# Optimization experiments

Hardware: AMD Instinct MI355X
Metric: run time of the kernel (lower is better)

## Reference

```python
import jax, jax.numpy as jnp
import numpy as np
import math

IN_FEATURES = 512
RFF_FEATURES = 2048
OUT_FEATURES = 1000
N = 8192
RIDGE_PENALTY = 1.0
MEAN_FIELD_FACTOR = 25.0
RFF_SCALAR = math.sqrt(RFF_FEATURES / 2)  # 32.0


def _random_ortho(key, n, m):
    q, _ = jnp.linalg.qr(jax.random.normal(key, (n, m), dtype=jnp.float32))
    return q


def setup_inputs() -> dict:
    key = jax.random.key(0)
    k_d, k_w, k_norm, k_b, k_lw, k_lb, k_cov = jax.random.split(key, 7)
    D = jax.random.normal(k_d, (N, IN_FEATURES), dtype=jnp.float32)
    # RFF weight: concat of random orthonormal blocks (rff_features > in_features)
    ws = []
    dim_left = RFF_FEATURES
    kk = k_w
    while dim_left > IN_FEATURES:
        kk, sub = jax.random.split(kk)
        ws.append(_random_ortho(sub, IN_FEATURES, IN_FEATURES))
        dim_left -= IN_FEATURES
    kk, sub = jax.random.split(kk)
    ws.append(_random_ortho(sub, IN_FEATURES, dim_left))
    W = jnp.concatenate(ws, axis=1)  # [in, rff]
    feature_norm = jax.random.normal(k_norm, W.shape, dtype=jnp.float32) ** 2
    W = W * jnp.sqrt(feature_norm.sum(0))
    b = jax.random.uniform(k_b, (RFF_FEATURES,), dtype=jnp.float32) * (2.0 * math.pi)
    # logit head (nn.Linear): weight [out, rff], bias [out]
    bound = 1.0 / math.sqrt(RFF_FEATURES)
    logit_w = jax.random.uniform(k_lw, (OUT_FEATURES, RFF_FEATURES), dtype=jnp.float32,
                                 minval=-bound, maxval=bound)
    logit_b = jax.random.uniform(k_lb, (OUT_FEATURES,), dtype=jnp.float32,
                                 minval=-bound, maxval=bound)
    # positive-definite covariance buffer (stand-in for inverted precision)
    A = jax.random.normal(k_cov, (RFF_FEATURES, RFF_FEATURES), dtype=jnp.float32) * 0.01
    covariance = A @ A.T + jnp.eye(RFF_FEATURES, dtype=jnp.float32)
    return {"D": D, "W": W, "b": b, "logit_w": logit_w, "logit_b": logit_b,
            "covariance": covariance}


def reference(D, W, b, logit_w, logit_b, covariance):
    # RFF feature map: cos(D @ W + b) / rff_scalar  -> [N, rff]
    Phi = jnp.cos(D @ W + b) / RFF_SCALAR
    # linear head -> [N, out]
    pred = Phi @ logit_w.T + logit_b
    # diag(Phi @ cov @ Phi.T) * ridge computed row-wise in O(N*r^2)
    diag_cov = jnp.sum((Phi @ covariance) * Phi, axis=-1) * RIDGE_PENALTY  # [N]
    logits_scale = jnp.sqrt(1.0 + diag_cov * MEAN_FIELD_FACTOR)
    return pred / logits_scale[:, None]
```

## Files before the change

kernel.cpp:

```cpp
#include <hip/hip_runtime.h>
#include <hip/hip_fp8.h>
#include <math.h>

#define N_ROWS 8192
#define IN_F   512
#define RFF    2048
#define OUT_F  1000
#define OUT_PAD 1024
#define INV_RFF_SCALAR 0.03125f
#define MEAN_FIELD 25.0f
#define PHI_NT 24

typedef __attribute__((ext_vector_type(8))) short short8;
typedef __attribute__((ext_vector_type(4))) float f32x4;
typedef __attribute__((ext_vector_type(2))) long long2v;

__device__ __forceinline__ unsigned short f32_to_bf16(float f) {
    unsigned u = __float_as_uint(f);
    unsigned r = 0x7FFFu + ((u >> 16) & 1u);
    return (unsigned short)((u + r) >> 16);
}
__device__ __forceinline__ float bf16_to_f32(unsigned short h) {
    return __uint_as_float(((unsigned)h) << 16);
}
__device__ __forceinline__ unsigned char f32_to_fp8(float x) {
    __hip_fp8_e4m3 q(x);
    return (unsigned char)q.__x;
}

__device__ __forceinline__ int perm64(int k) {
    return (k & ~63) | (((k >> 3) & 3) << 4) | (((k >> 5) & 1) << 3) | (k & 7);
}

__device__ __forceinline__ void stage_tile64(const unsigned short* __restrict__ X,
                                             int r0, int k0, unsigned char* lds,
                                             int w, int lane) {
    #pragma unroll
    for (int h = 0; h < 4; ++h) {
        int qb = h * 256 + w * 64;
        int q = qb + lane;
        int rt = q >> 7, c = (q >> 4) & 7, r = q & 15;
        const void* g = X + (size_t)(r0 + rt * 16 + r) * RFF + k0 + c * 8;
        __builtin_amdgcn_global_load_lds(
            (const __attribute__((address_space(1))) void*)g,
            (__attribute__((address_space(3))) void*)(lds + qb * 16),
            16, 0, 0);
    }
}

__device__ __forceinline__ void stage_tile8(const unsigned char* __restrict__ X,
                                            int r0, int k0b, unsigned char* lds,
                                            int w, int lane) {
    #pragma unroll
    for (int h = 0; h < 4; ++h) {
        int qb = h * 256 + w * 64;
        int q = qb + lane;
        int rt = q >> 7, c = (q >> 4) & 7, r = q & 15;
        const void* g = X + (size_t)(r0 + rt * 16 + r) * RFF + k0b + c * 16;
        __builtin_amdgcn_global_load_lds(
            (const __attribute__((address_space(1))) void*)g,
            (__attribute__((address_space(3))) void*)(lds + qb * 16),
            16, 0, 0);
    }
}

__global__ __launch_bounds__(256) void conv_split_kernel(
    const float* __restrict__ X, unsigned short* __restrict__ H,
    unsigned short* __restrict__ L, int n4)
{
    int i = blockIdx.x * 256 + threadIdx.x;
    if (i >= n4) return;
    float4 v = ((const float4*)X)[i];
    ushort4 h, l;
    h.x = f32_to_bf16(v.x); l.x = f32_to_bf16(v.x - bf16_to_f32(h.x));
    h.y = f32_to_bf16(v.y); l.y = f32_to_bf16(v.y - bf16_to_f32(h.y));
    h.z = f32_to_bf16(v.z); l.z = f32_to_bf16(v.z - bf16_to_f32(h.z));
    h.w = f32_to_bf16(v.w); l.w = f32_to_bf16(v.w - bf16_to_f32(h.w));
    ((ushort4*)H)[i] = h;
    ((ushort4*)L)[i] = l;
}

__global__ __launch_bounds__(256) void conv_covu8_kernel(
    const float* __restrict__ X, unsigned char* __restrict__ O)
{
    int i = blockIdx.x * 256 + threadIdx.x;
    int base = i * 4;
    int row = base >> 11;
    int col = base & 2047;
    int bn = row >> 7, bk = col >> 7;
    float w = (bk < bn) ? 16.0f : (bk == bn ? 8.0f : 0.0f);
    float4 v = ((const float4*)X)[i];
    float w0 = (col + 0 == row) ? 0.0f : w;
    float w1 = (col + 1 == row) ? 0.0f : w;
    float w2 = (col + 2 == row) ? 0.0f : w;
    float w3 = (col + 3 == row) ? 0.0f : w;
    uchar4 o;
    o.x = f32_to_fp8(v.x * w0); o.y = f32_to_fp8(v.y * w1);
    o.z = f32_to_fp8(v.z * w2); o.w = f32_to_fp8(v.w * w3);
    *(uchar4*)(O + (size_t)row * RFF + perm64(col)) = o;
}

__global__ __launch_bounds__(256) void conv_covd_kernel(
    const float* __restrict__ X, float* __restrict__ Cd)
{
    int i = blockIdx.x * 256 + threadIdx.x;
    if (i < RFF) Cd[i] = X[(size_t)i * RFF + i];
}

__global__ __launch_bounds__(256) void conv_phi8_kernel(
    const unsigned short* __restrict__ Phi16, unsigned char* __restrict__ Phi8)
{
    int i = blockIdx.x * 256 + threadIdx.x;
    int base = i * 4;
    int row = base >> 11;
    int col = base & 2047;
    ushort4 v = ((const ushort4*)Phi16)[i];
    uchar4 o;
    o.x = f32_to_fp8(bf16_to_f32(v.x) * 32.0f);
    o.y = f32_to_fp8(bf16_to_f32(v.y) * 32.0f);
    o.z = f32_to_fp8(bf16_to_f32(v.z) * 32.0f);
    o.w = f32_to_fp8(bf16_to_f32(v.w) * 32.0f);
    *(uchar4*)(Phi8 + (size_t)row * RFF + perm64(col)) = o;
}

__global__ __launch_bounds__(256) void conv_lw_kernel(
    const float* __restrict__ Lw, unsigned short* __restrict__ O)
{
    int i = blockIdx.x * 256 + threadIdx.x;
    int base = i * 4;
    int row = base >> 11;
    ushort4 o;
    if (row < OUT_F) {
        float4 v = ((const float4*)Lw)[i];
        o.x = f32_to_bf16(v.x); o.y = f32_to_bf16(v.y);
        o.z = f32_to_bf16(v.z); o.w = f32_to_bf16(v.w);
    } else {
        o.x = o.y = o.z = o.w = 0;
    }
    ((ushort4*)O)[i] = o;
}

__global__ __launch_bounds__(256) void conv_wt_kernel(
    const float* __restrict__ W, unsigned short* __restrict__ TH,
    unsigned short* __restrict__ TL)
{
    __shared__ float tile[64][65];
    const int tid = threadIdx.x;
    const int n0 = blockIdx.x * 64;
    const int k0 = blockIdx.y * 64;
    #pragma unroll
    for (int i = 0; i < 16; ++i) {
        int e = i * 256 + tid;
        int r = e >> 6, c = e & 63;
        tile[r][c] = W[(size_t)(k0 + r) * RFF + n0 + c];
    }
    __syncthreads();
    #pragma unroll
    for (int i = 0; i < 16; ++i) {
        int e = i * 256 + tid;
        int r = e >> 6, c = e & 63;
        float v = tile[c][r];
        unsigned short h = f32_to_bf16(v);
        unsigned short l = f32_to_bf16(v - bf16_to_f32(h));
        TH[(size_t)(n0 + r) * IN_F + k0 + c] = h;
        TL[(size_t)(n0 + r) * IN_F + k0 + c] = l;
    }
}


__device__ __forceinline__ void gload16u(const void* g, unsigned short* lds) {
    __builtin_amdgcn_global_load_lds(
        (const __attribute__((address_space(1))) void*)g,
        (__attribute__((address_space(3))) void*)lds, 16, 0, 0);
}

__device__ __forceinline__ void stageA_g(const unsigned short* __restrict__ src,
                                         int r0, int kk, unsigned short* ldsbuf,
                                         int Qa, int h, int w, int lane) {
    int q   = w * 64 + lane;
    int RTl = h * 8 + Qa * 4 + (q >> 7);
    int c   = (q >> 4) & 7, r = q & 15;
    const void* g = src + (size_t)(r0 + RTl * 16 + r) * IN_F + kk + c * 8;
    int RTu = h * 8 + Qa * 4 + (w >> 1);
    int cu  = (w & 1) * 4;
    gload16u(g, ldsbuf + RTu * 1024 + cu * 128);
}

__device__ __forceinline__ void stageB_g(const unsigned short* __restrict__ src,
                                         int cc0, int kk, unsigned short* ldsbuf,
                                         int nh, int h, int w, int lane) {
    int q    = w * 64 + lane;
    int i    = q >> 7;
    int RTp  = (i >> 1) * 4 + nh * 2 + (i & 1);
    int c    = (q >> 4) & 7, r = q & 15;
    const void* g = src + (size_t)(cc0 + h * 128 + RTp * 16 + r) * IN_F + kk + c * 8;
    int iu   = w >> 1;
    int RTpu = (iu >> 1) * 4 + nh * 2 + (iu & 1);
    int RTu  = h * 8 + RTpu;
    int cu   = (w & 1) * 4;
    gload16u(g, ldsbuf + RTu * 1024 + cu * 128);
}

#define SB0() __builtin_amdgcn_sched_barrier(0)
#define BARRIER() do { SB0(); __builtin_amdgcn_s_barrier(); SB0(); } while (0)
#define WAITVM(N) do { asm volatile("s_waitcnt vmcnt(" #N ")"); SB0(); } while (0)

#define READ_FA(FA, mh) do {                                                  \
    _Pragma("unroll")                                                         \
    for (int i_ = 0; i_ < 4; ++i_) {                                          \
        FA[i_][0] = *(const short8*)(A + (wm * 8 + (mh) * 4 + i_) * 1024      \
                                       + quad * 128 + ln * 8);                \
        FA[i_][1] = *(const short8*)(A + (wm * 8 + (mh) * 4 + i_) * 1024      \
                                       + 512 + quad * 128 + ln * 8);          \
    } } while (0)

#define READ_FB(FB, nh) do {                                                  \
    _Pragma("unroll")                                                         \
    for (int j_ = 0; j_ < 2; ++j_) {                                          \
        FB[j_][0] = *(const short8*)(B + (wn * 4 + (nh) * 2 + j_) * 1024      \
                                       + quad * 128 + ln * 8);                \
        FB[j_][1] = *(const short8*)(B + (wn * 4 + (nh) * 2 + j_) * 1024      \
                                       + 512 + quad * 128 + ln * 8);          \
    } } while (0)

#define MFMA16(MH, NH, FA, FB) do {                                           \
    __builtin_amdgcn_s_setprio(1);                                            \
    _Pragma("unroll")                                                         \
    for (int s_ = 0; s_ < 2; ++s_)                                            \
        _Pragma("unroll")                                                     \
        for (int i_ = 0; i_ < 4; ++i_)                                        \
            _Pragma("unroll")                                                 \
            for (int j_ = 0; j_ < 2; ++j_)                                    \
                acc[(MH) * 4 + i_][(NH) * 2 + j_] =                           \
                    __builtin_amdgcn_mfma_f32_16x16x32_bf16(                  \
                        FA[i_][s_], FB[j_][s_],                               \
                        acc[(MH) * 4 + i_][(NH) * 2 + j_], 0, 0, 0);          \
    __builtin_amdgcn_s_setprio(0);                                            \
} while (0)

__global__ __launch_bounds__(512, 2) void phi_mfma8p_kernel(
    const unsigned short* __restrict__ Dh, const unsigned short* __restrict__ Dl,
    const unsigned short* __restrict__ Wth, const unsigned short* __restrict__ Wtl,
    const float* __restrict__ bias, unsigned short* __restrict__ Phi)
{
    __shared__ unsigned short ldsA[2 * 16384];
    __shared__ unsigned short ldsB[2 * 16384];
    const int tid = threadIdx.x;
    const int w = tid >> 6, lane = tid & 63;
    const int wm = w >> 2, wn = w & 3;
    const int quad = lane >> 4, ln = lane & 15;

    const int bid = blockIdx.x;
    const int xcd = bid & 7, idx = bid >> 3;
    const int rb = (xcd >> 1) * 8 + (idx & 7);
    const int cb = (xcd & 1) * 4 + (idx >> 3);
    const int r0 = rb * 256;
    const int c0 = cb * 256;

    f32x4 acc[8][4];
    #pragma unroll
    for (int i = 0; i < 8; ++i)
        #pragma unroll
        for (int j = 0; j < 4; ++j)
            acc[i][j] = (f32x4)(0.0f);

    stageA_g(Dh,  r0, 0, ldsA, 0, 0, w, lane);
    stageA_g(Dh,  r0, 0, ldsA, 0, 1, w, lane);
    stageA_g(Dh,  r0, 0, ldsA, 1, 0, w, lane);
    stageA_g(Dh,  r0, 0, ldsA, 1, 1, w, lane);
    stageB_g(Wth, c0, 0, ldsB, 0, 0, w, lane);
    stageB_g(Wth, c0, 0, ldsB, 0, 1, w, lane);
    stageB_g(Wth, c0, 0, ldsB, 1, 0, w, lane);
    stageB_g(Wth, c0, 0, ldsB, 1, 1, w, lane);
    stageA_g(Dh,  r0, 64, ldsA + 16384, 0, 0, w, lane);
    stageA_g(Dh,  r0, 64, ldsA + 16384, 0, 1, w, lane);
    stageB_g(Wth, c0, 64, ldsB + 16384, 0, 0, w, lane);
    stageB_g(Wth, c0, 64, ldsB + 16384, 0, 1, w, lane);
    WAITVM(4);
    BARRIER();

    for (int t = 0; t < PHI_NT - 1; ++t) {
        const int buf = t & 1;
        const unsigned short* A = ldsA + buf * 16384;
        const unsigned short* B = ldsB + buf * 16384;
        unsigned short* curA = ldsA + buf * 16384;
        unsigned short* curB = ldsB + buf * 16384;
        unsigned short* othA = ldsA + (buf ^ 1) * 16384;
        unsigned short* othB = ldsB + (buf ^ 1) * 16384;
        const bool has2 = (t + 2) < PHI_NT;
        const int k1 = (t + 1) * 64, k2 = (t + 2) * 64;
        const int kk1 = k1 & 511, kk2 = k2 & 511;
        const unsigned short* A1 = (k1 >= 1024) ? Dl : Dh;
        const unsigned short* B1 = (k1 >= 1024) ? Wth : (k1 >= 512 ? Wtl : Wth);
        const unsigned short* A2 = (k2 >= 1024) ? Dl : Dh;
        const unsigned short* B2 = (k2 >= 1024) ? Wth : (k2 >= 512 ? Wtl : Wth);

        short8 fa[4][2], fb0[2][2], fb1[2][2];

        READ_FA(fa, 0);
        READ_FB(fb0, 0);
        stageA_g(A1, r0, kk1, othA, 1, 0, w, lane);
        stageA_g(A1, r0, kk1, othA, 1, 1, w, lane);
        BARRIER();
        MFMA16(0, 0, fa, fb0);
        BARRIER();

        READ_FB(fb1, 1);
        stageB_g(B1, c0, kk1, othB, 1, 0, w, lane);
        stageB_g(B1, c0, kk1, othB, 1, 1, w, lane);
        BARRIER();
        MFMA16(0, 1, fa, fb1);
        BARRIER();

        READ_FA(fa, 1);
        if (has2) { stageA_g(A2, r0, kk2, curA, 0, 0, w, lane);
                    stageA_g(A2, r0, kk2, curA, 0, 1, w, lane); }
        BARRIER();
        MFMA16(1, 0, fa, fb0);
        BARRIER();

        if (has2) { stageB_g(B2, c0, kk2, curB, 0, 0, w, lane);
                    stageB_g(B2, c0, kk2, curB, 0, 1, w, lane);
                    WAITVM(4); }
        else      { WAITVM(0); }
        BARRIER();
        MFMA16(1, 1, fa, fb1);
        BARRIER();
    }

    {
        asm volatile("" ::: "memory");
        const unsigned short* A = ldsA + ((PHI_NT - 1) & 1) * 16384;
        const unsigned short* B = ldsB + ((PHI_NT - 1) & 1) * 16384;
        short8 fa[4][2], fb0[2][2], fb1[2][2];
        READ_FA(fa, 0);
        READ_FB(fb0, 0);
        READ_FB(fb1, 1);
        MFMA16(0, 0, fa, fb0);
        MFMA16(0, 1, fa, fb1);
        READ_FA(fa, 1);
        MFMA16(1, 0, fa, fb0);
        MFMA16(1, 1, fa, fb1);
    }

    float bv[4];
    #pragma unroll
    for (int nt = 0; nt < 4; ++nt)
        bv[nt] = bias[c0 + wn * 64 + nt * 16 + ln];
    #pragma unroll
    for (int mt = 0; mt < 8; ++mt)
        #pragma unroll
        for (int nt = 0; nt < 4; ++nt) {
            int col = c0 + wn * 64 + nt * 16 + ln;
            #pragma unroll
            for (int reg = 0; reg < 4; ++reg) {
                int row = r0 + wm * 128 + mt * 16 + quad * 4 + reg;
                float z = acc[mt][nt][reg] + bv[nt];
                float p = __cosf(z) * INV_RFF_SCALAR;
                Phi[(size_t)row * RFF + col] = f32_to_bf16(p);
            }
        }
}

__global__ __launch_bounds__(256) void diag8_kernel(
    const unsigned char* __restrict__ Phi8, const unsigned char* __restrict__ CovU8,
    const unsigned short* __restrict__ Phi16, const float* __restrict__ Cd,
    float* __restrict__ diag)
{
    __shared__ __align__(16) unsigned char ldsA[16384];
    __shared__ __align__(16) unsigned char ldsB[16384];
    const int tid = threadIdx.x;
    const int w = tid >> 6, lane = tid & 63;
    const int wm = w >> 1, wn = w & 1;
    const int quad = lane >> 4, ln = lane & 15;
    const int J = 15 - blockIdx.x;
    const int r0 = blockIdx.y * 128;
    const int c0 = J * 128;
    const int kmax = (J + 1) * 128;

    f32x4 acc[4][4];
    #pragma unroll
    for (int i = 0; i < 4; ++i)
        #pragma unroll
        for (int j = 0; j < 4; ++j)
            acc[i][j] = (f32x4)(0.0f);

    for (int k0 = 0; k0 < kmax; k0 += 128) {
        __syncthreads();
        stage_tile8(Phi8,  r0, k0, ldsA, w, lane);
        stage_tile8(CovU8, c0, k0, ldsB, w, lane);
        __syncthreads();

        #pragma unroll
        for (int kb = 0; kb < 2; ++kb) {
            long2v fa[4], fb[4];
            #pragma unroll
            for (int t = 0; t < 4; ++t) {
                fa[t] = *(const long2v*)(ldsA + (((wm * 4 + t) * 128 + (kb * 4 + quad) * 16 + ln) << 4));
                fb[t] = *(const long2v*)(ldsB + (((wn * 4 + t) * 128 + (kb * 4 + quad) * 16 + ln) << 4));
            }
            #pragma unroll
            for (int mt = 0; mt < 4; ++mt)
                #pragma unroll
                for (int nt = 0; nt < 4; ++nt)
                    acc[mt][nt] = __builtin_amdgcn_mfma_f32_16x16x32_fp8_fp8(
                        fa[mt].x, fb[nt].x, acc[mt][nt], 0, 0, 0);
            #pragma unroll
            for (int mt = 0; mt < 4; ++mt)
                #pragma unroll
                for (int nt = 0; nt < 4; ++nt)
                    acc[mt][nt] = __builtin_amdgcn_mfma_f32_16x16x32_fp8_fp8(
                        fa[mt].y, fb[nt].y, acc[mt][nt], 0, 0, 0);
        }
    }

    float cd[4];
    #pragma unroll
    for (int nt = 0; nt < 4; ++nt)
        cd[nt] = 256.0f * Cd[c0 + wn * 64 + nt * 16 + ln];
    #pragma unroll
    for (int mt = 0; mt < 4; ++mt) {
        float psum[4] = {0.f, 0.f, 0.f, 0.f};
        #pragma unroll
        for (int nt = 0; nt < 4; ++nt) {
            int col = c0 + wn * 64 + nt * 16 + ln;
            #pragma unroll
            for (int reg = 0; reg < 4; ++reg) {
                int row = r0 + wm * 64 + mt * 16 + quad * 4 + reg;
                float pv = bf16_to_f32(Phi16[(size_t)row * RFF + col]);
                psum[reg] = fmaf(fmaf(cd[nt], pv, acc[mt][nt][reg]), pv, psum[reg]);
            }
        }
        #pragma unroll
        for (int off = 1; off < 16; off <<= 1)
            #pragma unroll
            for (int reg = 0; reg < 4; ++reg)
                psum[reg] += __shfl_xor(psum[reg], off, 16);
        if (ln == 0) {
            #pragma unroll
            for (int reg = 0; reg < 4; ++reg) {
                int row = r0 + wm * 64 + mt * 16 + quad * 4 + reg;
                atomicAdd(&diag[row], psum[reg] * (1.0f / 256.0f));
            }
        }
    }
}

__global__ __launch_bounds__(256) void pred_mfma_kernel(
    const unsigned short* __restrict__ Phi, const unsigned short* __restrict__ Lw,
    const float* __restrict__ Lb, const float* __restrict__ diag,
    float* __restrict__ out)
{
    __shared__ __align__(16) unsigned char ldsA[16384];
    __shared__ __align__(16) unsigned char ldsB[16384];
    const int tid = threadIdx.x;
    const int w = tid >> 6, lane = tid & 63;
    const int wm = w >> 1, wn = w & 1;
    const int quad = lane >> 4, ln = lane & 15;
    const int r0 = blockIdx.y * 128;
    const int c0 = blockIdx.x * 128;

    f32x4 acc[4][4];
    #pragma unroll
    for (int i = 0; i < 4; ++i)
        #pragma unroll
        for (int j = 0; j < 4; ++j)
            acc[i][j] = (f32x4)(0.0f);

    for (int k0 = 0; k0 < RFF; k0 += 64) {
        __syncthreads();
        stage_tile64(Phi, r0, k0, ldsA, w, lane);
        stage_tile64(Lw,  c0, k0, ldsB, w, lane);
        __syncthreads();

        #pragma unroll
        for (int s = 0; s < 2; ++s) {
            short8 fa[4], fb[4];
            #pragma unroll
            for (int t = 0; t < 4; ++t) {
                fa[t] = *(const short8*)(ldsA + (((wm * 4 + t) * 128 + (s * 4 + quad) * 16 + ln) << 4));
                fb[t] = *(const short8*)(ldsB + (((wn * 4 + t) * 128 + (s * 4 + quad) * 16 + ln) << 4));
            }
            #pragma unroll
            for (int mt = 0; mt < 4; ++mt)
                #pragma unroll
                for (int nt = 0; nt < 4; ++nt)
                    acc[mt][nt] = __builtin_amdgcn_mfma_f32_16x16x32_bf16(
                        fa[mt], fb[nt], acc[mt][nt], 0, 0, 0);
        }
    }

    #pragma unroll
    for (int mt = 0; mt < 4; ++mt) {
        float s[4];
        #pragma unroll
        for (int reg = 0; reg < 4; ++reg) {
            int row = r0 + wm * 64 + mt * 16 + quad * 4 + reg;
            s[reg] = 1.0f / sqrtf(1.0f + MEAN_FIELD * diag[row]);
        }
        #pragma unroll
        for (int nt = 0; nt < 4; ++nt) {
            int col = c0 + wn * 64 + nt * 16 + ln;
            if (col < OUT_F) {
                float bv = Lb[col];
                #pragma unroll
                for (int reg = 0; reg < 4; ++reg) {
                    int row = r0 + wm * 64 + mt * 16 + quad * 4 + reg;
                    out[(size_t)row * OUT_F + col] = (acc[mt][nt][reg] + bv) * s[reg];
                }
            }
        }
    }
}

extern "C" void kernel_launch(void* const* d_in, const int* in_sizes, int n_in,
                              void* d_out, int out_size, void* d_ws, size_t ws_size,
                              hipStream_t stream) {
    const float* D    = (const float*)d_in[0];
    const float* W    = (const float*)d_in[1];
    const float* bias = (const float*)d_in[2];
    const float* Lw   = (const float*)d_in[3];
    const float* Lb   = (const float*)d_in[4];
    const float* cov  = (const float*)d_in[5];
    float* out = (float*)d_out;

    char* p = (char*)d_ws;
    unsigned short* Phi16 = (unsigned short*)p;  p += (size_t)N_ROWS * RFF * 2;
    unsigned char*  Phi8  = (unsigned char*)p;
    unsigned short* Dh    = (unsigned short*)p;  p += (size_t)N_ROWS * IN_F * 2;
    unsigned short* Dl    = (unsigned short*)p;  p += (size_t)N_ROWS * IN_F * 2;
    unsigned short* Wth   = (unsigned short*)p;  p += (size_t)RFF * IN_F * 2;
    unsigned short* Wtl   = (unsigned short*)p;  p += (size_t)RFF * IN_F * 2;
    unsigned short* Lw16  = (unsigned short*)p;  p += (size_t)OUT_PAD * RFF * 2;
    unsigned char*  CovU8 = (unsigned char*)p;
    float*          Cd    = (float*)(p + (size_t)RFF * RFF);
    p += (size_t)RFF * RFF * 2;
    float* diag           = (float*)p;

    hipMemsetAsync(diag, 0, N_ROWS * sizeof(float), stream);

    dim3 blk(256);
    conv_split_kernel<<<dim3((N_ROWS * IN_F / 4 + 255) / 256), blk, 0, stream>>>(D, Dh, Dl, N_ROWS * IN_F / 4);
    conv_wt_kernel<<<dim3(RFF / 64, IN_F / 64), blk, 0, stream>>>(W, Wth, Wtl);
    conv_lw_kernel<<<dim3(OUT_PAD * RFF / 4 / 256), blk, 0, stream>>>(Lw, Lw16);
    conv_covu8_kernel<<<dim3(RFF * RFF / 4 / 256), blk, 0, stream>>>(cov, CovU8);
    conv_covd_kernel<<<dim3(RFF / 256), blk, 0, stream>>>(cov, Cd);

    phi_mfma8p_kernel<<<dim3(256), dim3(512), 0, stream>>>(Dh, Dl, Wth, Wtl, bias, Phi16);
    conv_phi8_kernel<<<dim3(N_ROWS * RFF / 4 / 256), blk, 0, stream>>>(Phi16, Phi8);

    diag8_kernel<<<dim3(16, N_ROWS / 128), blk, 0, stream>>>(Phi8, CovU8, Phi16, Cd, diag);
    pred_mfma_kernel<<<dim3(OUT_PAD / 128, N_ROWS / 128), blk, 0, stream>>>(Phi16, Lw16, Lb, diag, out);
}
```

Baseline: 313.7 us.

## Rewrite pred GEMM as 8-wave double-buffered pipelined kernel with XCD-aware tiling

Replaces the simple single-buffered 256-thread pred GEMM with a 512-thread, 256x128-tile kernel. It double-buffers LDS, interleaves the global-to-LDS loads for step t+2 with MFMA phases, and raises MFMA priority via setprio. Blocks are remapped so row tiles cluster per XCD for L2 reuse. The goal is to hide load latency and remove the two full syncthreads per k-step, at the cost of more complex scheduling and higher LDS use.

```diff
diff --git a/kernel.cpp b/kernel.cpp
--- a/kernel.cpp
+++ b/kernel.cpp
@@ -10,6 +10,7 @@
 #define INV_RFF_SCALAR 0.03125f
 #define MEAN_FIELD 25.0f
 #define PHI_NT 24
+#define PRED_NT 32
 
 typedef __attribute__((ext_vector_type(8))) short short8;
 typedef __attribute__((ext_vector_type(4))) float f32x4;
@@ -30,22 +31,6 @@
 
 __device__ __forceinline__ int perm64(int k) {
     return (k & ~63) | (((k >> 3) & 3) << 4) | (((k >> 5) & 1) << 3) | (k & 7);
-}
-
-__device__ __forceinline__ void stage_tile64(const unsigned short* __restrict__ X,
-                                             int r0, int k0, unsigned char* lds,
-                                             int w, int lane) {
-    #pragma unroll
-    for (int h = 0; h < 4; ++h) {
-        int qb = h * 256 + w * 64;
-        int q = qb + lane;
-        int rt = q >> 7, c = (q >> 4) & 7, r = q & 15;
-        const void* g = X + (size_t)(r0 + rt * 16 + r) * RFF + k0 + c * 8;
-        __builtin_amdgcn_global_load_lds(
-            (const __attribute__((address_space(1))) void*)g,
-            (__attribute__((address_space(3))) void*)(lds + qb * 16),
-            16, 0, 0);
-    }
 }
 
 __device__ __forceinline__ void stage_tile8(const unsigned char* __restrict__ X,
@@ -174,13 +159,14 @@
         (__attribute__((address_space(3))) void*)lds, 16, 0, 0);
 }
 
-__device__ __forceinline__ void stageA_g(const unsigned short* __restrict__ src,
-                                         int r0, int kk, unsigned short* ldsbuf,
+__device__ __forceinline__ void stage_ab(const unsigned short* __restrict__ src,
+                                         int stride, int r0v, int kk,
+                                         unsigned short* ldsbuf,
                                          int Qa, int h, int w, int lane) {
     int q   = w * 64 + lane;
-    int RTl = h * 8 + Qa * 4 + (q >> 7);
+    int RT  = h * 8 + Qa * 4 + (q >> 7);
     int c   = (q >> 4) & 7, r = q & 15;
-    const void* g = src + (size_t)(r0 + RTl * 16 + r) * IN_F + kk + c * 8;
+    const void* g = src + (size_t)(r0v + RT * 16 + r) * stride + kk + c * 8;
     int RTu = h * 8 + Qa * 4 + (w >> 1);
     int cu  = (w & 1) * 4;
     gload16u(g, ldsbuf + RTu * 1024 + cu * 128);
@@ -204,6 +190,7 @@
 #define SB0() __builtin_amdgcn_sched_barrier(0)
 #define BARRIER() do { SB0(); __builtin_amdgcn_s_barrier(); SB0(); } while (0)
 #define WAITVM(N) do { asm volatile("s_waitcnt vmcnt(" #N ")"); SB0(); } while (0)
+
 
 #define READ_FA(FA, mh) do {                                                  \
     _Pragma("unroll")                                                         \
@@ -264,16 +251,16 @@
         for (int j = 0; j < 4; ++j)
             acc[i][j] = (f32x4)(0.0f);
 
-    stageA_g(Dh,  r0, 0, ldsA, 0, 0, w, lane);
-    stageA_g(Dh,  r0, 0, ldsA, 0, 1, w, lane);
-    stageA_g(Dh,  r0, 0, ldsA, 1, 0, w, lane);
-    stageA_g(Dh,  r0, 0, ldsA, 1, 1, w, lane);
+    stage_ab(Dh, IN_F, r0, 0, ldsA, 0, 0, w, lane);
+    stage_ab(Dh, IN_F, r0, 0, ldsA, 0, 1, w, lane);
+    stage_ab(Dh, IN_F, r0, 0, ldsA, 1, 0, w, lane);
+    stage_ab(Dh, IN_F, r0, 0, ldsA, 1, 1, w, lane);
     stageB_g(Wth, c0, 0, ldsB, 0, 0, w, lane);
     stageB_g(Wth, c0, 0, ldsB, 0, 1, w, lane);
     stageB_g(Wth, c0, 0, ldsB, 1, 0, w, lane);
     stageB_g(Wth, c0, 0, ldsB, 1, 1, w, lane);
-    stageA_g(Dh,  r0, 64, ldsA + 16384, 0, 0, w, lane);
-    stageA_g(Dh,  r0, 64, ldsA + 16384, 0, 1, w, lane);
+    stage_ab(Dh, IN_F, r0, 64, ldsA + 16384, 0, 0, w, lane);
+    stage_ab(Dh, IN_F, r0, 64, ldsA + 16384, 0, 1, w, lane);
     stageB_g(Wth, c0, 64, ldsB + 16384, 0, 0, w, lane);
     stageB_g(Wth, c0, 64, ldsB + 16384, 0, 1, w, lane);
     WAITVM(4);
@@ -299,8 +286,8 @@
 
         READ_FA(fa, 0);
         READ_FB(fb0, 0);
-        stageA_g(A1, r0, kk1, othA, 1, 0, w, lane);
-        stageA_g(A1, r0, kk1, othA, 1, 1, w, lane);
+        stage_ab(A1, IN_F, r0, kk1, othA, 1, 0, w, lane);
+        stage_ab(A1, IN_F, r0, kk1, othA, 1, 1, w, lane);
         BARRIER();
         MFMA16(0, 0, fa, fb0);
         BARRIER();
@@ -313,8 +300,8 @@
         BARRIER();
 
         READ_FA(fa, 1);
-        if (has2) { stageA_g(A2, r0, kk2, curA, 0, 0, w, lane);
-                    stageA_g(A2, r0, kk2, curA, 0, 1, w, lane); }
+        if (has2) { stage_ab(A2, IN_F, r0, kk2, curA, 0, 0, w, lane);
+                    stage_ab(A2, IN_F, r0, kk2, curA, 0, 1, w, lane); }
         BARRIER();
         MFMA16(1, 0, fa, fb0);
         BARRIER();
@@ -446,19 +433,58 @@
     }
 }
 
-__global__ __launch_bounds__(256) void pred_mfma_kernel(
+
+#define READ_FA2(FA, mh) do {                                                 \
+    _Pragma("unroll")                                                         \
+    for (int i_ = 0; i_ < 2; ++i_) {                                          \
+        FA[i_][0] = *(const short8*)(A + (wm * 4 + (mh) * 2 + i_) * 1024      \
+                                       + quad * 128 + ln * 8);                \
+        FA[i_][1] = *(const short8*)(A + (wm * 4 + (mh) * 2 + i_) * 1024      \
+                                       + 512 + quad * 128 + ln * 8);          \
+    } } while (0)
+
+#define READ_FB2(FB, nh) do {                                                 \
+    _Pragma("unroll")                                                         \
+    for (int j_ = 0; j_ < 2; ++j_) {                                          \
+        FB[j_][0] = *(const short8*)(B + (wn * 4 + (nh) * 2 + j_) * 1024      \
+                                       + quad * 128 + ln * 8);                \
+        FB[j_][1] = *(const short8*)(B + (wn * 4 + (nh) * 2 + j_) * 1024      \
+                                       + 512 + quad * 128 + ln * 8);          \
+    } } while (0)
+
+#define MFMA8(MH, NH, FA, FB) do {                                            \
+    __builtin_amdgcn_s_setprio(1);                                            \
+    _Pragma("unroll")                                                         \
+    for (int s_ = 0; s_ < 2; ++s_)                                            \
+        _Pragma("unroll")                                                     \
+        for (int i_ = 0; i_ < 2; ++i_)                                        \
+            _Pragma("unroll")                                                 \
+            for (int j_ = 0; j_ < 2; ++j_)                                    \
+                acc[(MH) * 2 + i_][(NH) * 2 + j_] =                           \
+                    __builtin_amdgcn_mfma_f32_16x16x32_bf16(                  \
+                        FA[i_][s_], FB[j_][s_],                               \
+                        acc[(MH) * 2 + i_][(NH) * 2 + j_], 0, 0, 0);          \
+    __builtin_amdgcn_s_setprio(0);                                            \
+} while (0)
+
+__global__ __launch_bounds__(512, 2) void pred_mfma8p_kernel(
     const unsigned short* __restrict__ Phi, const unsigned short* __restrict__ Lw,
     const float* __restrict__ Lb, const float* __restrict__ diag,
     float* __restrict__ out)
 {
-    __shared__ __align__(16) unsigned char ldsA[16384];
-    __shared__ __align__(16) unsigned char ldsB[16384];
+    __shared__ unsigned short ldsA[2 * 16384];
+    __shared__ unsigned short ldsB[2 * 8192];
     const int tid = threadIdx.x;
     const int w = tid >> 6, lane = tid & 63;
     const int wm = w >> 1, wn = w & 1;
     const int quad = lane >> 4, ln = lane & 15;
-    const int r0 = blockIdx.y * 128;
-    const int c0 = blockIdx.x * 128;
+
+    const int bid = blockIdx.x;
+    const int xcd = bid & 7, idx = bid >> 3;
+    const int rb = xcd * 4 + (idx >> 3);
+    const int cb = idx & 7;
+    const int r0 = rb * 256;
+    const int c0 = cb * 128;
 
     f32x4 acc[4][4];
     #pragma unroll
@@ -467,27 +493,74 @@
         for (int j = 0; j < 4; ++j)
             acc[i][j] = (f32x4)(0.0f);
 
-    for (int k0 = 0; k0 < RFF; k0 += 64) {
-        __syncthreads();
-        stage_tile64(Phi, r0, k0, ldsA, w, lane);
-        stage_tile64(Lw,  c0, k0, ldsB, w, lane);
-        __syncthreads();
-
-        #pragma unroll
-        for (int s = 0; s < 2; ++s) {
-            short8 fa[4], fb[4];
-            #pragma unroll
-            for (int t = 0; t < 4; ++t) {
-                fa[t] = *(const short8*)(ldsA + (((wm * 4 + t) * 128 + (s * 4 + quad) * 16 + ln) << 4));
-                fb[t] = *(const short8*)(ldsB + (((wn * 4 + t) * 128 + (s * 4 + quad) * 16 + ln) << 4));
-            }
-            #pragma unroll
-            for (int mt = 0; mt < 4; ++mt)
-                #pragma unroll
-                for (int nt = 0; nt < 4; ++nt)
-                    acc[mt][nt] = __builtin_amdgcn_mfma_f32_16x16x32_bf16(
-                        fa[mt], fb[nt], acc[mt][nt], 0, 0, 0);
-        }
+    stage_ab(Phi, RFF, r0, 0, ldsA, 0, 0, w, lane);
+    stage_ab(Phi, RFF, r0, 0, ldsA, 1, 0, w, lane);
+    stage_ab(Phi, RFF, r0, 0, ldsA, 0, 1, w, lane);
+    stage_ab(Phi, RFF, r0, 0, ldsA, 1, 1, w, lane);
+    stage_ab(Lw,  RFF, c0, 0, ldsB, 0, 0, w, lane);
+    stage_ab(Lw,  RFF, c0, 0, ldsB, 1, 0, w, lane);
+    stage_ab(Phi, RFF, r0, 64, ldsA + 16384, 0, 0, w, lane);
+    stage_ab(Phi, RFF, r0, 64, ldsA + 16384, 1, 0, w, lane);
+    stage_ab(Phi, RFF, r0, 64, ldsA + 16384, 0, 1, w, lane);
+    stage_ab(Phi, RFF, r0, 64, ldsA + 16384, 1, 1, w, lane);
+    stage_ab(Lw,  RFF, c0, 64, ldsB + 8192, 0, 0, w, lane);
+    stage_ab(Lw,  RFF, c0, 64, ldsB + 8192, 1, 0, w, lane);
+    WAITVM(6);
+    BARRIER();
+
+    for (int t = 0; t < PRED_NT - 1; ++t) {
+        const int buf = t & 1;
+        const unsigned short* A = ldsA + buf * 16384;
+        const unsigned short* B = ldsB + buf * 8192;
+        unsigned short* curA = ldsA + buf * 16384;
+        unsigned short* curB = ldsB + buf * 8192;
+        const bool has2 = (t + 2) < PRED_NT;
+        const int kk2 = (t + 2) * 64;
+
+        short8 fa0[2][2], fa1[2][2], fb0[2][2], fb1[2][2];
+
+        READ_FA2(fa0, 0);
+        READ_FB2(fb0, 0);
+        BARRIER();
+        MFMA8(0, 0, fa0, fb0);
+        BARRIER();
+
+        READ_FB2(fb1, 1);
+        BARRIER();
+        MFMA8(0, 1, fa0, fb1);
+        BARRIER();
+
+        READ_FA2(fa1, 1);
+        if (has2) { stage_ab(Lw, RFF, c0, kk2, curB, 0, 0, w, lane);
+                    stage_ab(Lw, RFF, c0, kk2, curB, 1, 0, w, lane); }
+        BARRIER();
+        MFMA8(1, 0, fa1, fb0);
+        BARRIER();
+
+        if (has2) { stage_ab(Phi, RFF, r0, kk2, curA, 0, 0, w, lane);
+                    stage_ab(Phi, RFF, r0, kk2, curA, 1, 0, w, lane);
+                    stage_ab(Phi, RFF, r0, kk2, curA, 0, 1, w, lane);
+                    stage_ab(Phi, RFF, r0, kk2, curA, 1, 1, w, lane);
+                    WAITVM(6); }
+        else      { WAITVM(0); }
+        BARRIER();
+        MFMA8(1, 1, fa1, fb1);
+        BARRIER();
+    }
+
+    {
+        asm volatile("" ::: "memory");
+        const unsigned short* A = ldsA + ((PRED_NT - 1) & 1) * 16384;
+        const unsigned short* B = ldsB + ((PRED_NT - 1) & 1) * 8192;
+        short8 fa0[2][2], fa1[2][2], fb0[2][2], fb1[2][2];
+        READ_FA2(fa0, 0);
+        READ_FB2(fb0, 0);
+        READ_FB2(fb1, 1);
+        READ_FA2(fa1, 1);
+        MFMA8(0, 0, fa0, fb0);
+        MFMA8(0, 1, fa0, fb1);
+        MFMA8(1, 0, fa1, fb0);
+        MFMA8(1, 1, fa1, fb1);
     }
 
     #pragma unroll
@@ -550,5 +623,5 @@
     conv_phi8_kernel<<<dim3(N_ROWS * RFF / 4 / 256), blk, 0, stream>>>(Phi16, Phi8);
 
     diag8_kernel<<<dim3(16, N_ROWS / 128), blk, 0, stream>>>(Phi8, CovU8, Phi16, Cd, diag);
-    pred_mfma_kernel<<<dim3(OUT_PAD / 128, N_ROWS / 128), blk, 0, stream>>>(Phi16, Lw16, Lb, diag, out);
-}
+    pred_mfma8p_kernel<<<dim3(256), dim3(512), 0, stream>>>(Phi16, Lw16, Lb, diag, out);
+}
```

After: 325.8 us. +3.9%, slower.

## Double-buffer LDS staging in diag and pred GEMM kernels with XCD-aware tiling

Applied to the files above, without the earlier changes.

The diag8 kernel now double-buffers its fp8 tiles: it prefetches the next K tile into the alternate LDS buffer while the MFMAs run on the current one, and it raises wave priority around the MFMA block. The pred kernel is rewritten as a 512-thread, 256x128 tile kernel with double-buffered global_load_lds staging, a per-XCD block-to-tile mapping and priority hints. The aim is to hide global load latency and cut the two __syncthreads per iteration. The cost is doubled LDS per block and fewer concurrent blocks.

```diff
diff --git a/kernel.cpp b/kernel.cpp
--- a/kernel.cpp
+++ b/kernel.cpp
@@ -10,6 +10,7 @@
 #define INV_RFF_SCALAR 0.03125f
 #define MEAN_FIELD 25.0f
 #define PHI_NT 24
+#define PRED_NT 32
 
 typedef __attribute__((ext_vector_type(8))) short short8;
 typedef __attribute__((ext_vector_type(4))) float f32x4;
@@ -30,22 +31,6 @@
 
 __device__ __forceinline__ int perm64(int k) {
     return (k & ~63) | (((k >> 3) & 3) << 4) | (((k >> 5) & 1) << 3) | (k & 7);
-}
-
-__device__ __forceinline__ void stage_tile64(const unsigned short* __restrict__ X,
-                                             int r0, int k0, unsigned char* lds,
-                                             int w, int lane) {
-    #pragma unroll
-    for (int h = 0; h < 4; ++h) {
-        int qb = h * 256 + w * 64;
-        int q = qb + lane;
-        int rt = q >> 7, c = (q >> 4) & 7, r = q & 15;
-        const void* g = X + (size_t)(r0 + rt * 16 + r) * RFF + k0 + c * 8;
-        __builtin_amdgcn_global_load_lds(
-            (const __attribute__((address_space(1))) void*)g,
-            (__attribute__((address_space(3))) void*)(lds + qb * 16),
-            16, 0, 0);
-    }
 }
 
 __device__ __forceinline__ void stage_tile8(const unsigned char* __restrict__ X,
@@ -174,13 +159,14 @@
         (__attribute__((address_space(3))) void*)lds, 16, 0, 0);
 }
 
-__device__ __forceinline__ void stageA_g(const unsigned short* __restrict__ src,
-                                         int r0, int kk, unsigned short* ldsbuf,
+__device__ __forceinline__ void stage_ab(const unsigned short* __restrict__ src,
+                                         int stride, int r0v, int kk,
+                                         unsigned short* ldsbuf,
                                          int Qa, int h, int w, int lane) {
     int q   = w * 64 + lane;
-    int RTl = h * 8 + Qa * 4 + (q >> 7);
+    int RT  = h * 8 + Qa * 4 + (q >> 7);
     int c   = (q >> 4) & 7, r = q & 15;
-    const void* g = src + (size_t)(r0 + RTl * 16 + r) * IN_F + kk + c * 8;
+    const void* g = src + (size_t)(r0v + RT * 16 + r) * stride + kk + c * 8;
     int RTu = h * 8 + Qa * 4 + (w >> 1);
     int cu  = (w & 1) * 4;
     gload16u(g, ldsbuf + RTu * 1024 + cu * 128);
@@ -204,6 +190,7 @@
 #define SB0() __builtin_amdgcn_sched_barrier(0)
 #define BARRIER() do { SB0(); __builtin_amdgcn_s_barrier(); SB0(); } while (0)
 #define WAITVM(N) do { asm volatile("s_waitcnt vmcnt(" #N ")"); SB0(); } while (0)
+
 
 #define READ_FA(FA, mh) do {                                                  \
     _Pragma("unroll")                                                         \
@@ -264,16 +251,16 @@
         for (int j = 0; j < 4; ++j)
             acc[i][j] = (f32x4)(0.0f);
 
-    stageA_g(Dh,  r0, 0, ldsA, 0, 0, w, lane);
-    stageA_g(Dh,  r0, 0, ldsA, 0, 1, w, lane);
-    stageA_g(Dh,  r0, 0, ldsA, 1, 0, w, lane);
-    stageA_g(Dh,  r0, 0, ldsA, 1, 1, w, lane);
+    stage_ab(Dh, IN_F, r0, 0, ldsA, 0, 0, w, lane);
+    stage_ab(Dh, IN_F, r0, 0, ldsA, 0, 1, w, lane);
+    stage_ab(Dh, IN_F, r0, 0, ldsA, 1, 0, w, lane);
+    stage_ab(Dh, IN_F, r0, 0, ldsA, 1, 1, w, lane);
     stageB_g(Wth, c0, 0, ldsB, 0, 0, w, lane);
     stageB_g(Wth, c0, 0, ldsB, 0, 1, w, lane);
     stageB_g(Wth, c0, 0, ldsB, 1, 0, w, lane);
     stageB_g(Wth, c0, 0, ldsB, 1, 1, w, lane);
-    stageA_g(Dh,  r0, 64, ldsA + 16384, 0, 0, w, lane);
-    stageA_g(Dh,  r0, 64, ldsA + 16384, 0, 1, w, lane);
+    stage_ab(Dh, IN_F, r0, 64, ldsA + 16384, 0, 0, w, lane);
+    stage_ab(Dh, IN_F, r0, 64, ldsA + 16384, 0, 1, w, lane);
     stageB_g(Wth, c0, 64, ldsB + 16384, 0, 0, w, lane);
     stageB_g(Wth, c0, 64, ldsB + 16384, 0, 1, w, lane);
     WAITVM(4);
@@ -299,8 +286,8 @@
 
         READ_FA(fa, 0);
         READ_FB(fb0, 0);
-        stageA_g(A1, r0, kk1, othA, 1, 0, w, lane);
-        stageA_g(A1, r0, kk1, othA, 1, 1, w, lane);
+        stage_ab(A1, IN_F, r0, kk1, othA, 1, 0, w, lane);
+        stage_ab(A1, IN_F, r0, kk1, othA, 1, 1, w, lane);
         BARRIER();
         MFMA16(0, 0, fa, fb0);
         BARRIER();
@@ -313,8 +300,8 @@
         BARRIER();
 
         READ_FA(fa, 1);
-        if (has2) { stageA_g(A2, r0, kk2, curA, 0, 0, w, lane);
-                    stageA_g(A2, r0, kk2, curA, 0, 1, w, lane); }
+        if (has2) { stage_ab(A2, IN_F, r0, kk2, curA, 0, 0, w, lane);
+                    stage_ab(A2, IN_F, r0, kk2, curA, 0, 1, w, lane); }
         BARRIER();
         MFMA16(1, 0, fa, fb0);
         BARRIER();
@@ -362,13 +349,13 @@
         }
 }
 
-__global__ __launch_bounds__(256) void diag8_kernel(
+__global__ __launch_bounds__(256, 2) void diag8_kernel(
     const unsigned char* __restrict__ Phi8, const unsigned char* __restrict__ CovU8,
     const unsigned short* __restrict__ Phi16, const float* __restrict__ Cd,
     float* __restrict__ diag)
 {
-    __shared__ __align__(16) unsigned char ldsA[16384];
-    __shared__ __align__(16) unsigned char ldsB[16384];
+    __shared__ __align__(16) unsigned char ldsA[2 * 16384];
+    __shared__ __align__(16) unsigned char ldsB[2 * 16384];
     const int tid = threadIdx.x;
     const int w = tid >> 6, lane = tid & 63;
     const int wm = w >> 1, wn = w & 1;
@@ -385,19 +372,30 @@
         for (int j = 0; j < 4; ++j)
             acc[i][j] = (f32x4)(0.0f);
 
-    for (int k0 = 0; k0 < kmax; k0 += 128) {
-        __syncthreads();
-        stage_tile8(Phi8,  r0, k0, ldsA, w, lane);
-        stage_tile8(CovU8, c0, k0, ldsB, w, lane);
-        __syncthreads();
-
+    stage_tile8(Phi8,  r0, 0, ldsA, w, lane);
+    stage_tile8(CovU8, c0, 0, ldsB, w, lane);
+    WAITVM(0);
+    BARRIER();
+
+    int it = 0;
+    for (int k0 = 0; k0 < kmax; k0 += 128, ++it) {
+        const int buf = it & 1;
+        const unsigned char* A = ldsA + buf * 16384;
+        const unsigned char* B = ldsB + buf * 16384;
+
+        if (k0 + 128 < kmax) {
+            stage_tile8(Phi8,  r0, k0 + 128, ldsA + (buf ^ 1) * 16384, w, lane);
+            stage_tile8(CovU8, c0, k0 + 128, ldsB + (buf ^ 1) * 16384, w, lane);
+        }
+
+        __builtin_amdgcn_s_setprio(1);
         #pragma unroll
         for (int kb = 0; kb < 2; ++kb) {
             long2v fa[4], fb[4];
             #pragma unroll
             for (int t = 0; t < 4; ++t) {
-                fa[t] = *(const long2v*)(ldsA + (((wm * 4 + t) * 128 + (kb * 4 + quad) * 16 + ln) << 4));
-                fb[t] = *(const long2v*)(ldsB + (((wn * 4 + t) * 128 + (kb * 4 + quad) * 16 + ln) << 4));
+                fa[t] = *(const long2v*)(A + (((wm * 4 + t) * 128 + (kb * 4 + quad) * 16 + ln) << 4));
+                fb[t] = *(const long2v*)(B + (((wn * 4 + t) * 128 + (kb * 4 + quad) * 16 + ln) << 4));
             }
             #pragma unroll
             for (int mt = 0; mt < 4; ++mt)
@@ -412,6 +410,10 @@
                     acc[mt][nt] = __builtin_amdgcn_mfma_f32_16x16x32_fp8_fp8(
                         fa[mt].y, fb[nt].y, acc[mt][nt], 0, 0, 0);
         }
+        __builtin_amdgcn_s_setprio(0);
+
+        WAITVM(0);
+        BARRIER();
     }
 
     float cd[4];
@@ -446,19 +448,24 @@
     }
 }
 
-__global__ __launch_bounds__(256) void pred_mfma_kernel(
+__global__ __launch_bounds__(512, 2) void pred_min2_kernel(
     const unsigned short* __restrict__ Phi, const unsigned short* __restrict__ Lw,
     const float* __restrict__ Lb, const float* __restrict__ diag,
     float* __restrict__ out)
 {
-    __shared__ __align__(16) unsigned char ldsA[16384];
-    __shared__ __align__(16) unsigned char ldsB[16384];
+    __shared__ unsigned short ldsA[2 * 16384];
+    __shared__ unsigned short ldsB[2 * 8192];
     const int tid = threadIdx.x;
     const int w = tid >> 6, lane = tid & 63;
     const int wm = w >> 1, wn = w & 1;
     const int quad = lane >> 4, ln = lane & 15;
-    const int r0 = blockIdx.y * 128;
-    const int c0 = blockIdx.x * 128;
+
+    const int bid = blockIdx.x;
+    const int xcd = bid & 7, idx = bid >> 3;
+    const int rb = xcd * 4 + (idx >> 3);
+    const int cb = idx & 7;
+    const int r0 = rb * 256;
+    const int c0 = cb * 128;
 
     f32x4 acc[4][4];
     #pragma unroll
@@ -467,27 +474,56 @@
         for (int j = 0; j < 4; ++j)
             acc[i][j] = (f32x4)(0.0f);
 
-    for (int k0 = 0; k0 < RFF; k0 += 64) {
-        __syncthreads();
-        stage_tile64(Phi, r0, k0, ldsA, w, lane);
-        stage_tile64(Lw,  c0, k0, ldsB, w, lane);
-        __syncthreads();
-
-        #pragma unroll
-        for (int s = 0; s < 2; ++s) {
-            short8 fa[4], fb[4];
-            #pragma unroll
-            for (int t = 0; t < 4; ++t) {
-                fa[t] = *(const short8*)(ldsA + (((wm * 4 + t) * 128 + (s * 4 + quad) * 16 + ln) << 4));
-                fb[t] = *(const short8*)(ldsB + (((wn * 4 + t) * 128 + (s * 4 + quad) * 16 + ln) << 4));
-            }
-            #pragma unroll
-            for (int mt = 0; mt < 4; ++mt)
+    stage_ab(Phi, RFF, r0, 0, ldsA, 0, 0, w, lane);
+    stage_ab(Phi, RFF, r0, 0, ldsA, 1, 0, w, lane);
+    stage_ab(Phi, RFF, r0, 0, ldsA, 0, 1, w, lane);
+    stage_ab(Phi, RFF, r0, 0, ldsA, 1, 1, w, lane);
+    stage_ab(Lw,  RFF, c0, 0, ldsB, 0, 0, w, lane);
+    stage_ab(Lw,  RFF, c0, 0, ldsB, 1, 0, w, lane);
+    WAITVM(0);
+    BARRIER();
+
+    for (int t = 0; t < PRED_NT; ++t) {
+        const int buf = t & 1;
+        const unsigned short* A = ldsA + buf * 16384;
+        const unsigned short* B = ldsB + buf * 8192;
+
+        if (t + 1 < PRED_NT) {
+            const int kk = (t + 1) * 64;
+            unsigned short* nA = ldsA + (buf ^ 1) * 16384;
+            unsigned short* nB = ldsB + (buf ^ 1) * 8192;
+            stage_ab(Phi, RFF, r0, kk, nA, 0, 0, w, lane);
+            stage_ab(Phi, RFF, r0, kk, nA, 1, 0, w, lane);
+            stage_ab(Phi, RFF, r0, kk, nA, 0, 1, w, lane);
+            stage_ab(Phi, RFF, r0, kk, nA, 1, 1, w, lane);
+            stage_ab(Lw,  RFF, c0, kk, nB, 0, 0, w, lane);
+            stage_ab(Lw,  RFF, c0, kk, nB, 1, 0, w, lane);
+        }
+
+        short8 fa[4][2], fb[4][2];
+        #pragma unroll
+        for (int i_ = 0; i_ < 4; ++i_) {
+            fa[i_][0] = *(const short8*)(A + (wm * 4 + i_) * 1024 + quad * 128 + ln * 8);
+            fa[i_][1] = *(const short8*)(A + (wm * 4 + i_) * 1024 + 512 + quad * 128 + ln * 8);
+        }
+        #pragma unroll
+        for (int j_ = 0; j_ < 4; ++j_) {
+            fb[j_][0] = *(const short8*)(B + (wn * 4 + j_) * 1024 + quad * 128 + ln * 8);
+            fb[j_][1] = *(const short8*)(B + (wn * 4 + j_) * 1024 + 512 + quad * 128 + ln * 8);
+        }
+        __builtin_amdgcn_s_setprio(1);
+        #pragma unroll
+        for (int s_ = 0; s_ < 2; ++s_)
+            #pragma unroll
+            for (int i_ = 0; i_ < 4; ++i_)
                 #pragma unroll
-                for (int nt = 0; nt < 4; ++nt)
-                    acc[mt][nt] = __builtin_amdgcn_mfma_f32_16x16x32_bf16(
-                        fa[mt], fb[nt], acc[mt][nt], 0, 0, 0);
-        }
+                for (int j_ = 0; j_ < 4; ++j_)
+                    acc[i_][j_] = __builtin_amdgcn_mfma_f32_16x16x32_bf16(
+                        fa[i_][s_], fb[j_][s_], acc[i_][j_], 0, 0, 0);
+        __builtin_amdgcn_s_setprio(0);
+
+        WAITVM(0);
+        BARRIER();
     }
 
     #pragma unroll
@@ -550,5 +586,5 @@
     conv_phi8_kernel<<<dim3(N_ROWS * RFF / 4 / 256), blk, 0, stream>>>(Phi16, Phi8);
 
     diag8_kernel<<<dim3(16, N_ROWS / 128), blk, 0, stream>>>(Phi8, CovU8, Phi16, Cd, diag);
-    pred_mfma_kernel<<<dim3(OUT_PAD / 128, N_ROWS / 128), blk, 0, stream>>>(Phi16, Lw16, Lb, diag, out);
-}
+    pred_min2_kernel<<<dim3(256), dim3(512), 0, stream>>>(Phi16, Lw16, Lb, diag, out);
+}
```

New measurement: 317.3 us. About the same (+1.1%).
